# Kernel tuning notes

Hardware: AMD Instinct MI355X
Metric: run time of the kernel (lower is better)

## Reference

```python
import jax, jax.numpy as jnp
import numpy as np

H, DH = 8, 64  # num_heads, head_dim


def setup_inputs() -> dict:
    key = jax.random.key(0)
    ks = jax.random.split(key, 7)
    m, nq, nkv, d = 4, 2048, 2048, 512
    return {
        "xq": jax.random.normal(ks[0], (m, nq, d), jnp.float32),
        "xk": jax.random.normal(ks[1], (m, nkv, d), jnp.float32),
        "xv": jax.random.normal(ks[2], (m, nkv, d), jnp.float32),
        "Wq": jax.random.normal(ks[3], (d, H * DH), jnp.float32) * 0.02,
        "Wk": jax.random.normal(ks[4], (d, H * DH), jnp.float32) * 0.02,
        "Wv": jax.random.normal(ks[5], (d, H * DH), jnp.float32) * 0.02,
        "Wo": jax.random.normal(ks[6], (H * DH, d), jnp.float32) * 0.02,
        "bo": jnp.zeros((d,), jnp.float32),
    }


def _split_heads(t):
    # [b, n, h*d] -> [b, h, n, d]
    b, n, _ = t.shape
    return t.reshape(b, n, H, DH).transpose(0, 2, 1, 3)


def reference(xq, xk, xv, Wq, Wk, Wv, Wo, bo):
    scale = DH ** -0.5
    q = _split_heads(xq @ Wq)   # [b,h,nq,dh]
    k = _split_heads(xk @ Wk)   # [b,h,nkv,dh]
    v = _split_heads(xv @ Wv)   # [b,h,nkv,dh]
    dots = jnp.einsum("bhqd,bhkd->bhqk", q, k) * scale  # [b,h,nq,nkv]
    # diagonal attention term: query attends to its own (k,v) projection
    xq_k = _split_heads(xq @ Wk)
    xq_v = _split_heads(xq @ Wv)
    diag = jnp.sum(q * xq_k, axis=-1, keepdims=True) * scale  # [b,h,nq,1]
    dots = jnp.concatenate([dots, diag], axis=-1)  # [b,h,nq,nkv+1]
    attn = jax.nn.softmax(dots, axis=-1)
    out = jnp.einsum("bhqk,bhkd->bhqd", attn[..., :-1], v) + attn[..., -1:] * xq_v
    b, _, nq, _ = out.shape
    out = out.transpose(0, 2, 1, 3).reshape(b, nq, H * DH)  # merge heads
    return out @ Wo + bo
```

## Files before the change

kernel.cpp:

```cpp
#include <hip/hip_runtime.h>

#define LOG2E 1.44269504088896f
#define CS (0.125f * LOG2E)

typedef __bf16 bf16x8 __attribute__((ext_vector_type(8)));
typedef float f32x4 __attribute__((ext_vector_type(4)));
typedef unsigned short u16x8 __attribute__((ext_vector_type(8)));

#if __has_builtin(__builtin_amdgcn_exp2f)
#define fexp2(x) __builtin_amdgcn_exp2f(x)
#else
extern "C" __device__ float __ocml_native_exp2_f32(float);
#define fexp2(x) __ocml_native_exp2_f32(x)
#endif

__device__ __forceinline__ unsigned short f2bf(float f) {
  union { float f; unsigned int u; } v{f};
  unsigned int r = v.u + 0x7fffu + ((v.u >> 16) & 1u);
  return (unsigned short)(r >> 16);
}
__device__ __forceinline__ float bf2f(unsigned short u) {
  union { unsigned int u; float f; } v; v.u = ((unsigned int)u) << 16; return v.f;
}
__device__ __forceinline__ unsigned int pkr(float a, float b) {
  unsigned int ua = __builtin_bit_cast(unsigned int, a) + 0x8000u;
  unsigned int ub = __builtin_bit_cast(unsigned int, b) + 0x8000u;
  return __builtin_amdgcn_perm(ub, ua, 0x07060302);
}

typedef __attribute__((address_space(3))) unsigned int lds32_t;
typedef const __attribute__((address_space(1))) unsigned int glb32_t;
__device__ __forceinline__ void gld16(const unsigned short* g, unsigned short* l) {
  __builtin_amdgcn_global_load_lds((glb32_t*)(unsigned long long)g,
                                   (lds32_t*)(unsigned int)(unsigned long long)l,
                                   16, 0, 0);
}

__global__ __launch_bounds__(256) void conv_all(
    const float* __restrict__ xq, const float* __restrict__ xk, const float* __restrict__ xv,
    const float* __restrict__ Wq, const float* __restrict__ Wk,
    const float* __restrict__ Wv, const float* __restrict__ Wo,
    unsigned short* __restrict__ oxq, unsigned short* __restrict__ oxk, unsigned short* __restrict__ oxv,
    unsigned short* __restrict__ oWq, unsigned short* __restrict__ oWk,
    unsigned short* __restrict__ oWv, unsigned short* __restrict__ oWo) {
  __shared__ unsigned short T[64 * 65];
  const int blk = blockIdx.x;
  if (blk < 12288) {
    const int N4 = (8192 * 512) / 4;
    int idx = blk * 256 + threadIdx.x;
    const float* src; unsigned short* dst; int i;
    if (idx < N4)          { src = xq; dst = oxq; i = idx; }
    else if (idx < 2 * N4) { src = xk; dst = oxk; i = idx - N4; }
    else                   { src = xv; dst = oxv; i = idx - 2 * N4; }
    float4 v = ((const float4*)src)[i];
    ushort4 o; o.x = f2bf(v.x); o.y = f2bf(v.y); o.z = f2bf(v.z); o.w = f2bf(v.w);
    ((ushort4*)dst)[i] = o;
  } else {
    const int wblk = blk - 12288;
    const int wsel = wblk >> 6;
    const int tile = wblk & 63;
    const int tk = (tile >> 3) * 64, tn = (tile & 7) * 64;
    const float* src = (wsel == 0) ? Wq : (wsel == 1) ? Wk : (wsel == 2) ? Wv : Wo;
    unsigned short* dst = (wsel == 0) ? oWq : (wsel == 1) ? oWk : (wsel == 2) ? oWv : oWo;
    const float scale = (wsel == 0) ? CS : 1.0f;
    const int rr = threadIdx.x >> 4;
    const int cc = (threadIdx.x & 15) * 4;
#pragma unroll
    for (int i = 0; i < 4; i++) {
      int row = rr + i * 16;
      float4 v = *(const float4*)&src[(size_t)(tk + row) * 512 + tn + cc];
      T[(cc + 0) * 65 + row] = f2bf(v.x * scale);
      T[(cc + 1) * 65 + row] = f2bf(v.y * scale);
      T[(cc + 2) * 65 + row] = f2bf(v.z * scale);
      T[(cc + 3) * 65 + row] = f2bf(v.w * scale);
    }
    __syncthreads();
#pragma unroll
    for (int i = 0; i < 4; i++) {
      int n = rr + i * 16;
      ushort4 o;
      o.x = T[n * 65 + cc + 0]; o.y = T[n * 65 + cc + 1];
      o.z = T[n * 65 + cc + 2]; o.w = T[n * 65 + cc + 3];
      *(ushort4*)&dst[(size_t)(tn + n) * 512 + tk + cc] = o;
    }
  }
}

__device__ __forceinline__ void gemm_tile(
    const unsigned short* __restrict__ A, const unsigned short* __restrict__ Bt,
    int rowBlk, int colBlk, unsigned short* As, unsigned short* Bs, f32x4 (&acc)[4][4]) {
  const int t = threadIdx.x;
  const int lane = t & 63, c = lane & 15, g = lane >> 4;
  const int w = t >> 6;
  const int wm = w & 1, wn = w >> 1;
#pragma unroll
  for (int i = 0; i < 4; i++)
#pragma unroll
    for (int j = 0; j < 4; j++)
#pragma unroll
      for (int r = 0; r < 4; r++) acc[i][j][r] = 0.f;

  for (int kk = 0; kk < 512; kk += 32) {
    __syncthreads();
#pragma unroll
    for (int i = 0; i < 2; i++) {
      int idx = t + 256 * i;
      int r = idx >> 2, ch = idx & 3;
      gld16(&A[(size_t)(rowBlk + r) * 512 + kk + ch * 8], &As[idx * 8]);
      gld16(&Bt[(size_t)(colBlk + r) * 512 + kk + ch * 8], &Bs[idx * 8]);
    }
    __syncthreads();
    bf16x8 af[4], bfr[4];
#pragma unroll
    for (int i = 0; i < 4; i++)
      af[i] = __builtin_bit_cast(bf16x8, *(const u16x8*)&As[(wm * 64 + i * 16 + c) * 32 + g * 8]);
#pragma unroll
    for (int j = 0; j < 4; j++)
      bfr[j] = __builtin_bit_cast(bf16x8, *(const u16x8*)&Bs[(wn * 64 + j * 16 + c) * 32 + g * 8]);
#pragma unroll
    for (int i = 0; i < 4; i++)
#pragma unroll
      for (int j = 0; j < 4; j++)
        acc[i][j] = __builtin_amdgcn_mfma_f32_16x16x32_bf16(af[i], bfr[j], acc[i][j], 0, 0, 0);
  }
}

__global__ __launch_bounds__(256) void proj_all(
    const unsigned short* __restrict__ xq, const unsigned short* __restrict__ xk,
    const unsigned short* __restrict__ xv,
    const unsigned short* __restrict__ Wq, const unsigned short* __restrict__ Wk,
    const unsigned short* __restrict__ Wv,
    unsigned short* __restrict__ Qo, unsigned short* __restrict__ XKo,
    unsigned short* __restrict__ XVo, unsigned short* __restrict__ Ko,
    unsigned short* __restrict__ Vto) {
  __shared__ unsigned short As[128 * 32];
  __shared__ unsigned short Bs[128 * 32];
  const int rowBlk = blockIdx.x * 128;
  const int y = blockIdx.y;
  const unsigned short* A; const unsigned short* Bt; int colBlk; int mode;
  unsigned short* out;
  if (y < 12) {
    int wsel = y >> 2;
    A = xq; colBlk = (y & 3) * 128; mode = 0;
    Bt = (wsel == 0) ? Wq : (wsel == 1) ? Wk : Wv;
    out = (wsel == 0) ? Qo : (wsel == 1) ? XKo : XVo;
  } else if (y < 16) {
    A = xk; Bt = Wk; out = Ko; colBlk = (y - 12) * 128; mode = 0;
  } else {
    A = xv; Bt = Wv; out = Vto; colBlk = (y - 16) * 128; mode = 1;
  }
  f32x4 acc[4][4];
  gemm_tile(A, Bt, rowBlk, colBlk, As, Bs, acc);
  const int t = threadIdx.x;
  const int w = t >> 6, lane = t & 63, c = lane & 15, g = lane >> 4;
  const int wm = w & 1, wn = w >> 1;
  if (mode == 0) {
#pragma unroll
    for (int i = 0; i < 4; i++)
#pragma unroll
      for (int j = 0; j < 4; j++)
#pragma unroll
        for (int r = 0; r < 4; r++) {
          int row = rowBlk + wm * 64 + i * 16 + g * 4 + r;
          int col = colBlk + wn * 64 + j * 16 + c;
          out[(size_t)row * 512 + col] = f2bf(acc[i][j][r]);
        }
  } else {
#pragma unroll
    for (int i = 0; i < 4; i++) {
      int tok0 = rowBlk + wm * 64 + i * 16 + g * 4;
      int bb = tok0 >> 11, n0 = tok0 & 2047;
#pragma unroll
      for (int j = 0; j < 4; j++) {
        int col = colBlk + wn * 64 + j * 16 + c;
        int hh = col >> 6, dh = col & 63;
        ushort4 o;
        o.x = f2bf(acc[i][j][0]); o.y = f2bf(acc[i][j][1]);
        o.z = f2bf(acc[i][j][2]); o.w = f2bf(acc[i][j][3]);
        *(ushort4*)&out[((size_t)(bb * 8 + hh) * 64 + dh) * 2048 + n0] = o;
      }
    }
  }
}

__global__ __launch_bounds__(256) void gemm_out(
    const unsigned short* __restrict__ A, const unsigned short* __restrict__ Bt,
    float* __restrict__ out, const float* __restrict__ bias) {
  __shared__ unsigned short As[128 * 32];
  __shared__ unsigned short Bs[64 * 32];
  const int rowBlk = blockIdx.x * 128;
  const int colBlk = blockIdx.y * 64;
  const int t = threadIdx.x;
  const int lane = t & 63, c = lane & 15, g = lane >> 4;
  const int w = t >> 6;
  const int wm = w & 1, wn = w >> 1;
  f32x4 acc[4][2];
#pragma unroll
  for (int i = 0; i < 4; i++)
#pragma unroll
    for (int j = 0; j < 2; j++)
#pragma unroll
      for (int r = 0; r < 4; r++) acc[i][j][r] = 0.f;

  for (int kk = 0; kk < 512; kk += 32) {
    __syncthreads();
#pragma unroll
    for (int i = 0; i < 2; i++) {
      int idx = t + 256 * i;
      int r = idx >> 2, ch = idx & 3;
      gld16(&A[(size_t)(rowBlk + r) * 512 + kk + ch * 8], &As[idx * 8]);
    }
    {
      int r = t >> 2, ch = t & 3;
      gld16(&Bt[(size_t)(colBlk + r) * 512 + kk + ch * 8], &Bs[t * 8]);
    }
    __syncthreads();
    bf16x8 af[4], bfr[2];
#pragma unroll
    for (int i = 0; i < 4; i++)
      af[i] = __builtin_bit_cast(bf16x8, *(const u16x8*)&As[(wm * 64 + i * 16 + c) * 32 + g * 8]);
#pragma unroll
    for (int j = 0; j < 2; j++)
      bfr[j] = __builtin_bit_cast(bf16x8, *(const u16x8*)&Bs[(wn * 32 + j * 16 + c) * 32 + g * 8]);
#pragma unroll
    for (int i = 0; i < 4; i++)
#pragma unroll
      for (int j = 0; j < 2; j++)
        acc[i][j] = __builtin_amdgcn_mfma_f32_16x16x32_bf16(af[i], bfr[j], acc[i][j], 0, 0, 0);
  }
#pragma unroll
  for (int i = 0; i < 4; i++)
#pragma unroll
    for (int j = 0; j < 2; j++)
#pragma unroll
      for (int r = 0; r < 4; r++) {
        int row = rowBlk + wm * 64 + i * 16 + g * 4 + r;
        int col = colBlk + wn * 32 + j * 16 + c;
        out[(size_t)row * 512 + col] = acc[i][j][r] + bias[col];
      }
}

__global__ __launch_bounds__(512, 4) void attn_kernel(
    const unsigned short* __restrict__ Q, const unsigned short* __restrict__ K,
    const unsigned short* __restrict__ Vt, const unsigned short* __restrict__ XK,
    const unsigned short* __restrict__ XV, unsigned short* __restrict__ O) {
  __shared__ unsigned short Ks[2][64 * 64];
  __shared__ unsigned short Vs[3][64 * 64];
  __shared__ unsigned short Ps[2][8][16 * 72];
  __shared__ float Scr[8][32];
  const int t = threadIdx.x;
  const int w = t >> 6, lane = t & 63, c = lane & 15, g = lane >> 4;
  const int qt = blockIdx.x, h = blockIdx.y, b = blockIdx.z;
  const size_t hb = (size_t)b * (2048 * 512) + h * 64;
  const size_t vhb = (size_t)(b * 8 + h) * 64 * 2048;
  const int qbase = qt * 128 + w * 16;

  const int sr = t >> 3, sch = t & 7;
  const int ssl = (sch ^ (sr & 7)) * 8;
  const size_t kgoff = hb + (size_t)sr * 512 + ssl;
  const size_t vgoff = vhb + (size_t)sr * 2048 + ssl;

  const int sw0 = ((g ^ (c & 7)) << 3);
  const int sw1 = (((g | 4) ^ (c & 7)) << 3);

  bf16x8 qf[2];
#pragma unroll
  for (int hf = 0; hf < 2; hf++)
    qf[hf] = __builtin_bit_cast(bf16x8,
        *(const u16x8*)&Q[hb + (size_t)(qbase + c) * 512 + hf * 32 + g * 8]);

  f32x4 accO[4];
  float lq = 0.f;
#pragma unroll
  for (int jd = 0; jd < 4; jd++)
#pragma unroll
    for (int r = 0; r < 4; r++) accO[jd][r] = 0.f;

  gld16(&K[kgoff], &Ks[0][t * 8]);
  gld16(&Vt[vgoff], &Vs[0][t * 8]);
  __syncthreads();

  gld16(&K[kgoff + (size_t)(64 * 512)], &Ks[1][t * 8]);
  gld16(&Vt[vgoff + 64], &Vs[1][t * 8]);
  {
    unsigned short* Pw = &Ps[0][w][0];
    f32x4 s[4];
    __builtin_amdgcn_s_setprio(1);
#pragma unroll
    for (int j = 0; j < 4; j++) {
      bf16x8 kf0 = __builtin_bit_cast(bf16x8, *(const u16x8*)&Ks[0][(j * 16 + c) * 64 + sw0]);
      bf16x8 kf1 = __builtin_bit_cast(bf16x8, *(const u16x8*)&Ks[0][(j * 16 + c) * 64 + sw1]);
      f32x4 z; z[0] = z[1] = z[2] = z[3] = 0.f;
      z = __builtin_amdgcn_mfma_f32_16x16x32_bf16(kf0, qf[0], z, 0, 0, 0);
      z = __builtin_amdgcn_mfma_f32_16x16x32_bf16(kf1, qf[1], z, 0, 0, 0);
      s[j] = z;
    }
    __builtin_amdgcn_s_setprio(0);
    float sum = 0.f;
#pragma unroll
    for (int j = 0; j < 4; j++) {
      float p0 = fexp2(s[j][0]);
      float p1 = fexp2(s[j][1]);
      float p2 = fexp2(s[j][2]);
      float p3 = fexp2(s[j][3]);
      sum += (p0 + p1) + (p2 + p3);
      uint2 pw; pw.x = pkr(p0, p1); pw.y = pkr(p2, p3);
      *(uint2*)&Pw[c * 72 + j * 16 + g * 4] = pw;
    }
    lq += sum;
  }
  __syncthreads();

  int vprev = 0, vcur = 1, vnext = 2;
  for (int kt = 1; kt < 32; kt++) {
    if (kt < 31) {
      gld16(&K[kgoff + (size_t)(kt + 1) * (64 * 512)], &Ks[(kt + 1) & 1][t * 8]);
      gld16(&Vt[vgoff + (size_t)(kt + 1) * 64], &Vs[vnext][t * 8]);
    }
    const unsigned short* Pp = &Ps[(kt - 1) & 1][w][0];
    bf16x8 pf0 = __builtin_bit_cast(bf16x8, *(const u16x8*)&Pp[c * 72 + g * 8]);
    bf16x8 pf1 = __builtin_bit_cast(bf16x8, *(const u16x8*)&Pp[c * 72 + 32 + g * 8]);

    const unsigned short* Kc = &Ks[kt & 1][0];
    f32x4 s[4];
    __builtin_amdgcn_s_setprio(1);
#pragma unroll
    for (int j = 0; j < 4; j++) {
      bf16x8 kf0 = __builtin_bit_cast(bf16x8, *(const u16x8*)&Kc[(j * 16 + c) * 64 + sw0]);
      bf16x8 kf1 = __builtin_bit_cast(bf16x8, *(const u16x8*)&Kc[(j * 16 + c) * 64 + sw1]);
      f32x4 z; z[0] = z[1] = z[2] = z[3] = 0.f;
      z = __builtin_amdgcn_mfma_f32_16x16x32_bf16(kf0, qf[0], z, 0, 0, 0);
      z = __builtin_amdgcn_mfma_f32_16x16x32_bf16(kf1, qf[1], z, 0, 0, 0);
      s[j] = z;
    }
    const unsigned short* Vc = &Vs[vprev][0];
#pragma unroll
    for (int jd = 0; jd < 4; jd++) {
      bf16x8 v0 = __builtin_bit_cast(bf16x8, *(const u16x8*)&Vc[(jd * 16 + c) * 64 + sw0]);
      bf16x8 v1 = __builtin_bit_cast(bf16x8, *(const u16x8*)&Vc[(jd * 16 + c) * 64 + sw1]);
      accO[jd] = __builtin_amdgcn_mfma_f32_16x16x32_bf16(pf0, v0, accO[jd], 0, 0, 0);
      accO[jd] = __builtin_amdgcn_mfma_f32_16x16x32_bf16(pf1, v1, accO[jd], 0, 0, 0);
    }
    __builtin_amdgcn_s_setprio(0);

    {
      unsigned short* Pw = &Ps[kt & 1][w][0];
      float sum = 0.f;
#pragma unroll
      for (int j = 0; j < 4; j++) {
        float p0 = fexp2(s[j][0]);
        float p1 = fexp2(s[j][1]);
        float p2 = fexp2(s[j][2]);
        float p3 = fexp2(s[j][3]);
        sum += (p0 + p1) + (p2 + p3);
        uint2 pw; pw.x = pkr(p0, p1); pw.y = pkr(p2, p3);
        *(uint2*)&Pw[c * 72 + j * 16 + g * 4] = pw;
      }
      lq += sum;
    }

    if (kt < 31) __syncthreads();
    int tmp = vprev; vprev = vcur; vcur = vnext; vnext = tmp;
  }

  {
    const unsigned short* Pp = &Ps[1][w][0];
    bf16x8 pf0 = __builtin_bit_cast(bf16x8, *(const u16x8*)&Pp[c * 72 + g * 8]);
    bf16x8 pf1 = __builtin_bit_cast(bf16x8, *(const u16x8*)&Pp[c * 72 + 32 + g * 8]);
    const unsigned short* Vc = &Vs[vprev][0];
    __builtin_amdgcn_s_setprio(1);
#pragma unroll
    for (int jd = 0; jd < 4; jd++) {
      bf16x8 v0 = __builtin_bit_cast(bf16x8, *(const u16x8*)&Vc[(jd * 16 + c) * 64 + sw0]);
      bf16x8 v1 = __builtin_bit_cast(bf16x8, *(const u16x8*)&Vc[(jd * 16 + c) * 64 + sw1]);
      accO[jd] = __builtin_amdgcn_mfma_f32_16x16x32_bf16(pf0, v0, accO[jd], 0, 0, 0);
      accO[jd] = __builtin_amdgcn_mfma_f32_16x16x32_bf16(pf1, v1, accO[jd], 0, 0, 0);
    }
    __builtin_amdgcn_s_setprio(0);
  }

  lq += __shfl_xor(lq, 16);
  lq += __shfl_xor(lq, 32);

  {
    const int qc = qbase + c;
    float part = 0.f;
    {
      const unsigned short* qp = &Q[hb + (size_t)qc * 512 + g * 16];
      const unsigned short* xp = &XK[hb + (size_t)qc * 512 + g * 16];
      u16x8 q0 = *(const u16x8*)&qp[0], q1 = *(const u16x8*)&qp[8];
      u16x8 x0 = *(const u16x8*)&xp[0], x1 = *(const u16x8*)&xp[8];
#pragma unroll
      for (int ii = 0; ii < 8; ii++)
        part += bf2f(q0[ii]) * bf2f(x0[ii]) + bf2f(q1[ii]) * bf2f(x1[ii]);
    }
    part += __shfl_xor(part, 16);
    part += __shfl_xor(part, 32);
    float pd = fexp2(part);
    float inv = 1.f / (lq + pd);
    if (g == 0) {
      Scr[w][c] = inv;
      Scr[w][16 + c] = pd * inv;
    }
    __builtin_amdgcn_s_waitcnt(0);
    f32x4 a4 = *(const f32x4*)&Scr[w][g * 4];
    f32x4 p4 = *(const f32x4*)&Scr[w][16 + g * 4];
#pragma unroll
    for (int jd = 0; jd < 4; jd++)
#pragma unroll
      for (int r = 0; r < 4; r++) {
        int qr = qbase + g * 4 + r;
        float xv = bf2f(XV[hb + (size_t)qr * 512 + jd * 16 + c]);
        float val = accO[jd][r] * a4[r] + p4[r] * xv;
        O[((size_t)(b * 2048 + qr)) * 512 + h * 64 + jd * 16 + c] = f2bf(val);
      }
  }
}

extern "C" void kernel_launch(void* const* d_in, const int* in_sizes, int n_in,
                              void* d_out, int out_size, void* d_ws, size_t ws_size,
                              hipStream_t stream) {
  const float* xq = (const float*)d_in[0];
  const float* xk = (const float*)d_in[1];
  const float* xv = (const float*)d_in[2];
  const float* Wq = (const float*)d_in[3];
  const float* Wk = (const float*)d_in[4];
  const float* Wv = (const float*)d_in[5];
  const float* Wo = (const float*)d_in[6];
  const float* bo = (const float*)d_in[7];

  unsigned short* ws = (unsigned short*)d_ws;
  const size_t MD = 8192ull * 512;
  const size_t WD = 512ull * 512;
  unsigned short* xq_b = ws;
  unsigned short* xk_b = xq_b + MD;
  unsigned short* xv_b = xk_b + MD;
  unsigned short* Wq_t = xv_b + MD;
  unsigned short* Wk_t = Wq_t + WD;
  unsigned short* Wv_t = Wk_t + WD;
  unsigned short* Wo_t = Wv_t + WD;
  unsigned short* Qb  = Wo_t + WD;
  unsigned short* Kb  = Qb + MD;
  unsigned short* Vtb = Kb + MD;
  unsigned short* XKb = Vtb + MD;
  unsigned short* XVb = XKb + MD;
  unsigned short* Ob  = XVb + MD;

  conv_all<<<dim3(12544), 256, 0, stream>>>(xq, xk, xv, Wq, Wk, Wv, Wo,
                                            xq_b, xk_b, xv_b, Wq_t, Wk_t, Wv_t, Wo_t);
  proj_all<<<dim3(64, 20), 256, 0, stream>>>(xq_b, xk_b, xv_b, Wq_t, Wk_t, Wv_t,
                                             Qb, XKb, XVb, Kb, Vtb);
  attn_kernel<<<dim3(16, 8, 4), 512, 0, stream>>>(Qb, Kb, Vtb, XKb, XVb, Ob);
  gemm_out<<<dim3(64, 8), 256, 0, stream>>>(Ob, Wo_t, (float*)d_out, bo);
}
```

Before: 201.6 us.

## Double-buffer LDS in projection GEMMs and remap attention blocks by head

```diff
diff --git a/kernel.cpp b/kernel.cpp
--- a/kernel.cpp
+++ b/kernel.cpp
@@ -100,29 +100,41 @@
 #pragma unroll
       for (int r = 0; r < 4; r++) acc[i][j][r] = 0.f;
 
-  for (int kk = 0; kk < 512; kk += 32) {
-    __syncthreads();
-#pragma unroll
-    for (int i = 0; i < 2; i++) {
-      int idx = t + 256 * i;
-      int r = idx >> 2, ch = idx & 3;
-      gld16(&A[(size_t)(rowBlk + r) * 512 + kk + ch * 8], &As[idx * 8]);
-      gld16(&Bt[(size_t)(colBlk + r) * 512 + kk + ch * 8], &Bs[idx * 8]);
-    }
-    __syncthreads();
+  const int sr = t >> 2, sch = t & 3;
+#define STAGE_PROJ(kkk, buf)                                                     \
+  do {                                                                           \
+    unsigned short* Ad = As + (buf) * (128 * 32);                                \
+    unsigned short* Bd = Bs + (buf) * (128 * 32);                                \
+    gld16(&A[(size_t)(rowBlk + sr) * 512 + (kkk) + sch * 8], &Ad[t * 8]);        \
+    gld16(&Bt[(size_t)(colBlk + sr) * 512 + (kkk) + sch * 8], &Bd[t * 8]);       \
+    gld16(&A[(size_t)(rowBlk + sr + 64) * 512 + (kkk) + sch * 8],                \
+          &Ad[(t + 256) * 8]);                                                   \
+    gld16(&Bt[(size_t)(colBlk + sr + 64) * 512 + (kkk) + sch * 8],               \
+          &Bd[(t + 256) * 8]);                                                   \
+  } while (0)
+
+  STAGE_PROJ(0, 0);
+  __syncthreads();
+
+  for (int kt = 0; kt < 16; kt++) {
+    if (kt < 15) STAGE_PROJ((kt + 1) * 32, (kt + 1) & 1);
+    const unsigned short* Ac = As + (kt & 1) * (128 * 32);
+    const unsigned short* Bc = Bs + (kt & 1) * (128 * 32);
     bf16x8 af[4], bfr[4];
 #pragma unroll
     for (int i = 0; i < 4; i++)
-      af[i] = __builtin_bit_cast(bf16x8, *(const u16x8*)&As[(wm * 64 + i * 16 + c) * 32 + g * 8]);
+      af[i] = __builtin_bit_cast(bf16x8, *(const u16x8*)&Ac[(wm * 64 + i * 16 + c) * 32 + g * 8]);
 #pragma unroll
     for (int j = 0; j < 4; j++)
-      bfr[j] = __builtin_bit_cast(bf16x8, *(const u16x8*)&Bs[(wn * 64 + j * 16 + c) * 32 + g * 8]);
+      bfr[j] = __builtin_bit_cast(bf16x8, *(const u16x8*)&Bc[(wn * 64 + j * 16 + c) * 32 + g * 8]);
 #pragma unroll
     for (int i = 0; i < 4; i++)
 #pragma unroll
       for (int j = 0; j < 4; j++)
         acc[i][j] = __builtin_amdgcn_mfma_f32_16x16x32_bf16(af[i], bfr[j], acc[i][j], 0, 0, 0);
-  }
+    if (kt < 15) __syncthreads();
+  }
+#undef STAGE_PROJ
 }
 
 __global__ __launch_bounds__(256) void proj_all(
@@ -133,8 +145,8 @@
     unsigned short* __restrict__ Qo, unsigned short* __restrict__ XKo,
     unsigned short* __restrict__ XVo, unsigned short* __restrict__ Ko,
     unsigned short* __restrict__ Vto) {
-  __shared__ unsigned short As[128 * 32];
-  __shared__ unsigned short Bs[128 * 32];
+  __shared__ unsigned short As[2 * 128 * 32];
+  __shared__ unsigned short Bs[2 * 128 * 32];
   const int rowBlk = blockIdx.x * 128;
   const int y = blockIdx.y;
   const unsigned short* A; const unsigned short* Bt; int colBlk; int mode;
@@ -186,8 +198,8 @@
 __global__ __launch_bounds__(256) void gemm_out(
     const unsigned short* __restrict__ A, const unsigned short* __restrict__ Bt,
     float* __restrict__ out, const float* __restrict__ bias) {
-  __shared__ unsigned short As[128 * 32];
-  __shared__ unsigned short Bs[64 * 32];
+  __shared__ unsigned short As[2 * 128 * 32];
+  __shared__ unsigned short Bs[2 * 64 * 32];
   const int rowBlk = blockIdx.x * 128;
   const int colBlk = blockIdx.y * 64;
   const int t = threadIdx.x;
@@ -202,32 +214,39 @@
 #pragma unroll
       for (int r = 0; r < 4; r++) acc[i][j][r] = 0.f;
 
-  for (int kk = 0; kk < 512; kk += 32) {
-    __syncthreads();
-#pragma unroll
-    for (int i = 0; i < 2; i++) {
-      int idx = t + 256 * i;
-      int r = idx >> 2, ch = idx & 3;
-      gld16(&A[(size_t)(rowBlk + r) * 512 + kk + ch * 8], &As[idx * 8]);
-    }
-    {
-      int r = t >> 2, ch = t & 3;
-      gld16(&Bt[(size_t)(colBlk + r) * 512 + kk + ch * 8], &Bs[t * 8]);
-    }
-    __syncthreads();
+  const int sr = t >> 2, sch = t & 3;
+#define STAGE_OUT(kkk, buf)                                                      \
+  do {                                                                           \
+    unsigned short* Ad = As + (buf) * (128 * 32);                                \
+    unsigned short* Bd = Bs + (buf) * (64 * 32);                                 \
+    gld16(&A[(size_t)(rowBlk + sr) * 512 + (kkk) + sch * 8], &Ad[t * 8]);        \
+    gld16(&A[(size_t)(rowBlk + sr + 64) * 512 + (kkk) + sch * 8],                \
+          &Ad[(t + 256) * 8]);                                                   \
+    gld16(&Bt[(size_t)(colBlk + sr) * 512 + (kkk) + sch * 8], &Bd[t * 8]);       \
+  } while (0)
+
+  STAGE_OUT(0, 0);
+  __syncthreads();
+
+  for (int kt = 0; kt < 16; kt++) {
+    if (kt < 15) STAGE_OUT((kt + 1) * 32, (kt + 1) & 1);
+    const unsigned short* Ac = As + (kt & 1) * (128 * 32);
+    const unsigned short* Bc = Bs + (kt & 1) * (64 * 32);
     bf16x8 af[4], bfr[2];
 #pragma unroll
     for (int i = 0; i < 4; i++)
-      af[i] = __builtin_bit_cast(bf16x8, *(const u16x8*)&As[(wm * 64 + i * 16 + c) * 32 + g * 8]);
+      af[i] = __builtin_bit_cast(bf16x8, *(const u16x8*)&Ac[(wm * 64 + i * 16 + c) * 32 + g * 8]);
 #pragma unroll
     for (int j = 0; j < 2; j++)
-      bfr[j] = __builtin_bit_cast(bf16x8, *(const u16x8*)&Bs[(wn * 32 + j * 16 + c) * 32 + g * 8]);
+      bfr[j] = __builtin_bit_cast(bf16x8, *(const u16x8*)&Bc[(wn * 32 + j * 16 + c) * 32 + g * 8]);
 #pragma unroll
     for (int i = 0; i < 4; i++)
 #pragma unroll
       for (int j = 0; j < 2; j++)
         acc[i][j] = __builtin_amdgcn_mfma_f32_16x16x32_bf16(af[i], bfr[j], acc[i][j], 0, 0, 0);
-  }
+    if (kt < 15) __syncthreads();
+  }
+#undef STAGE_OUT
 #pragma unroll
   for (int i = 0; i < 4; i++)
 #pragma unroll
@@ -250,7 +269,11 @@
   __shared__ float Scr[8][32];
   const int t = threadIdx.x;
   const int w = t >> 6, lane = t & 63, c = lane & 15, g = lane >> 4;
-  const int qt = blockIdx.x, h = blockIdx.y, b = blockIdx.z;
+  const int id = blockIdx.x + 16 * (blockIdx.y + 8 * blockIdx.z);
+  const int h = id & 7;
+  const int jj = id >> 3;
+  const int qt = jj & 15;
+  const int b = jj >> 4;
   const size_t hb = (size_t)b * (2048 * 512) + h * 64;
   const size_t vhb = (size_t)(b * 8 + h) * 64 * 2048;
   const int qbase = qt * 128 + w * 16;
```

Measured after the change: 202.4 us. About the same (+0.4%).
